# Performance work log

Measured on AMD Instinct MI355X. Metric: run time of the kernel, lower is better.

Reference implementation:

```python
import jax, jax.numpy as jnp
import numpy as np

HEAD_DIM = 8


def setup_inputs() -> dict:
    key = jax.random.key(0)
    kq, kk, k1, k2, k3, k4 = jax.random.split(key, 6)
    B, C, D, H, W = 2, 64, 32, 64, 64
    query_feats = jax.random.normal(kq, (B, C, D, H, W), dtype=jnp.float32)
    key_feats = jax.random.normal(kk, (B, C, D, H, W), dtype=jnp.float32)
    s = 1.0 / np.sqrt(C)
    # 1x1x1 Conv3d (bias=False) weights, stored as [out_ch, in_ch]
    Wq = jax.random.normal(k1, (C, C), dtype=jnp.float32) * s
    Wk = jax.random.normal(k2, (C, C), dtype=jnp.float32) * s
    Wv = jax.random.normal(k3, (C, C), dtype=jnp.float32) * s
    Wo = jax.random.normal(k4, (C, C), dtype=jnp.float32) * s
    return {"query_feats": query_feats, "key_feats": key_feats,
            "Wq": Wq, "Wk": Wk, "Wv": Wv, "Wo": Wo}


def _proj(W, x):
    # 1x1x1 conv == channel mixing
    return jnp.einsum('oc,bcdhw->bodhw', W, x)


def reference(query_feats, key_feats, Wq, Wk, Wv, Wo):
    B, C, D, H, W_ = query_feats.shape
    hw = H * W_
    heads = C // HEAD_DIM
    q = _proj(Wq, query_feats)   # [B, C, D, H, W]
    k = _proj(Wk, key_feats)
    v = _proj(Wv, key_feats)
    # reshape to [B, heads, head_dim, D, hw] then rearrange
    q = q.reshape(B, heads, HEAD_DIM, D, hw).transpose(0, 4, 1, 3, 2)  # [B,hw,heads,D,hd]
    k = k.reshape(B, heads, HEAD_DIM, D, hw).transpose(0, 4, 1, 2, 3)  # [B,hw,heads,hd,D]
    v = v.reshape(B, heads, HEAD_DIM, D, hw).transpose(0, 4, 1, 3, 2)  # [B,hw,heads,D,hd]
    sim = jnp.matmul(q, k) * (HEAD_DIM ** -0.5)      # [B,hw,heads,D,D]
    sim = jax.nn.softmax(sim, axis=-1)
    ctx = jnp.matmul(sim, v)                          # [B,hw,heads,D,hd]
    # permute(0,1,2,4,3) then flatten heads*hd -> C, then to [B,C,D,H,W]
    ctx = ctx.transpose(0, 1, 2, 4, 3).reshape(B, hw, C, D)
    ctx = ctx.transpose(0, 2, 3, 1).reshape(B, C, D, H, W_)
    out = _proj(Wo, ctx)
    return out
```

## Files before the change

### kernel.cpp

```cpp
#include <hip/hip_runtime.h>

#define SB   131072
#define CSTR 131072
#define BSTR 8388608

using u32x4  = __attribute__((ext_vector_type(4))) unsigned int;
using u32x2  = __attribute__((ext_vector_type(2))) unsigned int;
using bf16x8 = __attribute__((ext_vector_type(8))) short;
using f32x4  = __attribute__((ext_vector_type(4))) float;
using f32x2  = __attribute__((ext_vector_type(2))) float;

__device__ __forceinline__ unsigned pack2(float a, float b) {
    unsigned r;
    asm("v_cvt_pk_bf16_f32 %0, %1, %2" : "=v"(r) : "v"(a), "v"(b));
    return r;
}
__device__ __forceinline__ float bflo(unsigned u) { return __uint_as_float(u << 16); }
__device__ __forceinline__ float bfhi(unsigned u) { return __uint_as_float(u & 0xffff0000u); }

__device__ __forceinline__ f32x4 mfma16(bf16x8 a, bf16x8 b, f32x4 c) {
    return __builtin_amdgcn_mfma_f32_16x16x32_bf16(a, b, c, 0, 0, 0);
}

#define LOAD_A_FRAGS(A, W, n, qd)                                          \
    _Pragma("unroll")                                                      \
    for (int mt = 0; mt < 4; ++mt) {                                       \
        _Pragma("unroll")                                                  \
        for (int kt = 0; kt < 2; ++kt) {                                   \
            union { bf16x8 v; unsigned u[4]; } tw;                         \
            _Pragma("unroll")                                              \
            for (int r = 0; r < 4; ++r) {                                  \
                const int o = mt * 16 + (n);                               \
                const int c = kt * 32 + (qd) * 8 + 2 * r;                  \
                const float2 wv = *(const float2*)&W[o * 64 + c];          \
                tw.u[r] = pack2(wv.x, wv.y);                               \
            }                                                              \
            A[mt][kt] = tw.v;                                              \
        }                                                                  \
    }

__global__ __launch_bounds__(256)
void k1_proj(const float* __restrict__ qf, const float* __restrict__ kf,
             const float* __restrict__ Wq, const float* __restrict__ Wk,
             const float* __restrict__ Wv, unsigned* __restrict__ Qs,
             unsigned* __restrict__ Ks, unsigned* __restrict__ Vs)
{
    const int vbid = blockIdx.x >> 1;
    const int path = blockIdx.x & 1;
    const int wid  = (vbid * 256 + (int)threadIdx.x) >> 6;
    const int lane = threadIdx.x & 63;
    const int qd   = lane >> 4;
    const int n    = lane & 15;
    const int S0   = wid * 64;
    const int b    = S0 >> 17;
    const int tl   = S0 & (SB - 1);

    if (path == 0) {
        const float* xb = qf + (size_t)b * BSTR;
        bf16x8 A[4][2];
        LOAD_A_FRAGS(A, Wq, n, qd)

        #pragma unroll
        for (int t = 0; t < 4; ++t) {
            const int site = tl + t * 16 + n;
            bf16x8 Bf[2];
            #pragma unroll
            for (int kt = 0; kt < 2; ++kt) {
                union { bf16x8 v; unsigned u[4]; } tb;
                #pragma unroll
                for (int r = 0; r < 4; ++r) {
                    const int c = kt * 32 + qd * 8 + 2 * r;
                    tb.u[r] = pack2(xb[(size_t)c * CSTR + site],
                                    xb[(size_t)(c + 1) * CSTR + site]);
                }
                Bf[kt] = tb.v;
            }
            f32x4 acc[4];
            #pragma unroll
            for (int mt = 0; mt < 4; ++mt) acc[mt] = (f32x4){0.f, 0.f, 0.f, 0.f};
            #pragma unroll
            for (int kt = 0; kt < 2; ++kt)
                #pragma unroll
                for (int mt = 0; mt < 4; ++mt)
                    acc[mt] = mfma16(A[mt][kt], Bf[kt], acc[mt]);
            #pragma unroll
            for (int mt = 0; mt < 4; ++mt) {
                const int h = 2 * mt + (qd >> 1);
                unsigned* dst = Qs + ((unsigned)(b * 8 + h) * SB + site) * 4 + (qd & 1) * 2;
                u32x2 w;
                w.x = pack2(acc[mt][0], acc[mt][1]);
                w.y = pack2(acc[mt][2], acc[mt][3]);
                *(u32x2*)dst = w;
            }
        }
    } else {
        const float* xb = kf + (size_t)b * BSTR;
        bf16x8 AK[4][2], AV[4][2];
        LOAD_A_FRAGS(AK, Wk, n, qd)
        LOAD_A_FRAGS(AV, Wv, n, qd)

        #pragma unroll
        for (int t = 0; t < 4; ++t) {
            const int site = tl + t * 16 + n;
            bf16x8 Bf[2];
            #pragma unroll
            for (int kt = 0; kt < 2; ++kt) {
                union { bf16x8 v; unsigned u[4]; } tb;
                #pragma unroll
                for (int r = 0; r < 4; ++r) {
                    const int c = kt * 32 + qd * 8 + 2 * r;
                    tb.u[r] = pack2(xb[(size_t)c * CSTR + site],
                                    xb[(size_t)(c + 1) * CSTR + site]);
                }
                Bf[kt] = tb.v;
            }
            f32x4 aK[4], aV[4];
            #pragma unroll
            for (int mt = 0; mt < 4; ++mt) {
                aK[mt] = (f32x4){0.f, 0.f, 0.f, 0.f};
                aV[mt] = (f32x4){0.f, 0.f, 0.f, 0.f};
            }
            #pragma unroll
            for (int kt = 0; kt < 2; ++kt)
                #pragma unroll
                for (int mt = 0; mt < 4; ++mt) {
                    aK[mt] = mfma16(AK[mt][kt], Bf[kt], aK[mt]);
                    aV[mt] = mfma16(AV[mt][kt], Bf[kt], aV[mt]);
                }
            #pragma unroll
            for (int mt = 0; mt < 4; ++mt) {
                const int h = 2 * mt + (qd >> 1);
                const unsigned off = ((unsigned)(b * 8 + h) * SB + site) * 4 + (qd & 1) * 2;
                u32x2 wk2, wv2;
                wk2.x = pack2(aK[mt][0], aK[mt][1]);
                wk2.y = pack2(aK[mt][2], aK[mt][3]);
                wv2.x = pack2(aV[mt][0], aV[mt][1]);
                wv2.y = pack2(aV[mt][2], aV[mt][3]);
                *(u32x2*)(Ks + off) = wk2;
                *(u32x2*)(Vs + off) = wv2;
            }
        }
    }
}

__global__ __launch_bounds__(256)
void k2_attn(const u32x4* Qs, const u32x4* __restrict__ Ks,
             const u32x4* __restrict__ Vs, u32x4* Cs)
{
    __shared__ unsigned int kls[4096];
    __shared__ unsigned int vls[4096];

    const int blk = blockIdx.x;
    const int h   = blk & 7;
    const int w   = blk >> 3;
    const int b   = w >> 7;
    const int pos0 = (w & 127) * 32;

    const int tid = threadIdx.x;
    const int pos = tid & 31;
    const int dqt = tid >> 5;

    const int base = (b * 8 + h) * SB;

    #pragma unroll
    for (int i = 0; i < 4; ++i) {
        const int idx = tid + i * 256;
        const int dp = idx >> 5, pp = idx & 31;
        *(u32x4*)&kls[idx * 4] = Ks[base + dp * 4096 + pos0 + pp];
        *(u32x4*)&vls[idx * 4] = Vs[base + dp * 4096 + pos0 + pp];
    }
    __syncthreads();

    const float sc = 0.35355339059327373f * 1.4426950408889634f;

    #pragma unroll 1
    for (int p = 0; p < 2; ++p) {
        const int dq0 = dqt + 16 * p;
        const u32x4 qa = Qs[base + dq0 * 4096 + pos0 + pos];
        const u32x4 qb = Qs[base + (dq0 + 8) * 4096 + pos0 + pos];
        f32x2 q2[8];
        q2[0] = (f32x2){bflo(qa.x) * sc, bflo(qb.x) * sc};
        q2[1] = (f32x2){bfhi(qa.x) * sc, bfhi(qb.x) * sc};
        q2[2] = (f32x2){bflo(qa.y) * sc, bflo(qb.y) * sc};
        q2[3] = (f32x2){bfhi(qa.y) * sc, bfhi(qb.y) * sc};
        q2[4] = (f32x2){bflo(qa.z) * sc, bflo(qb.z) * sc};
        q2[5] = (f32x2){bfhi(qa.z) * sc, bfhi(qb.z) * sc};
        q2[6] = (f32x2){bflo(qa.w) * sc, bflo(qb.w) * sc};
        q2[7] = (f32x2){bfhi(qa.w) * sc, bfhi(qb.w) * sc};

        f32x2 cx[8];
        #pragma unroll
        for (int e = 0; e < 8; ++e) cx[e] = (f32x2){0.f, 0.f};
        f32x2 sum2 = (f32x2){0.f, 0.f};

        #pragma unroll 4
        for (int dp = 0; dp < 32; ++dp) {
            const u32x4 kk = *(const u32x4*)&kls[(dp * 32 + pos) * 4];
            const u32x4 vv = *(const u32x4*)&vls[(dp * 32 + pos) * 4];
            f32x2 accA = q2[0] * bflo(kk.x);
            f32x2 accB = q2[1] * bfhi(kk.x);
            accA += q2[2] * bflo(kk.y);
            accB += q2[3] * bfhi(kk.y);
            accA += q2[4] * bflo(kk.z);
            accB += q2[5] * bfhi(kk.z);
            accA += q2[6] * bflo(kk.w);
            accB += q2[7] * bfhi(kk.w);
            const f32x2 acc = accA + accB;
            f32x2 ex;
            ex.x = exp2f(acc.x);
            ex.y = exp2f(acc.y);
            sum2 += ex;
            cx[0] += ex * bflo(vv.x);
            cx[1] += ex * bfhi(vv.x);
            cx[2] += ex * bflo(vv.y);
            cx[3] += ex * bfhi(vv.y);
            cx[4] += ex * bflo(vv.z);
            cx[5] += ex * bfhi(vv.z);
            cx[6] += ex * bflo(vv.w);
            cx[7] += ex * bfhi(vv.w);
        }

        const f32x2 inv2 = (f32x2){1.0f / sum2.x, 1.0f / sum2.y};
        #pragma unroll
        for (int e = 0; e < 8; ++e) cx[e] *= inv2;

        u32x4 pa, pb;
        pa.x = pack2(cx[0].x, cx[1].x); pa.y = pack2(cx[2].x, cx[3].x);
        pa.z = pack2(cx[4].x, cx[5].x); pa.w = pack2(cx[6].x, cx[7].x);
        pb.x = pack2(cx[0].y, cx[1].y); pb.y = pack2(cx[2].y, cx[3].y);
        pb.z = pack2(cx[4].y, cx[5].y); pb.w = pack2(cx[6].y, cx[7].y);
        Cs[base + dq0 * 4096 + pos0 + pos] = pa;
        Cs[base + (dq0 + 8) * 4096 + pos0 + pos] = pb;
    }
}

__global__ __launch_bounds__(256)
void k3_out(const u32x4* __restrict__ Cs, const float* __restrict__ Wo,
            float* __restrict__ out)
{
    const int wid  = (blockIdx.x * 256 + threadIdx.x) >> 6;
    const int lane = threadIdx.x & 63;
    const int qd   = lane >> 4;
    const int n    = lane & 15;
    const int S0   = wid * 64;
    const int b    = S0 >> 17;
    const int tl   = S0 & (SB - 1);

    bf16x8 A[4][2];
    LOAD_A_FRAGS(A, Wo, n, qd)

    #pragma unroll
    for (int t = 0; t < 4; ++t) {
        const int site = tl + t * 16 + n;
        bf16x8 Bf[2];
        #pragma unroll
        for (int kt = 0; kt < 2; ++kt) {
            Bf[kt] = *(const bf16x8*)(Cs + (unsigned)(b * 8 + kt * 4 + qd) * SB + site);
        }
        f32x4 acc[4];
        #pragma unroll
        for (int mt = 0; mt < 4; ++mt) acc[mt] = (f32x4){0.f, 0.f, 0.f, 0.f};
        #pragma unroll
        for (int kt = 0; kt < 2; ++kt)
            #pragma unroll
            for (int mt = 0; mt < 4; ++mt)
                acc[mt] = mfma16(A[mt][kt], Bf[kt], acc[mt]);
        #pragma unroll
        for (int mt = 0; mt < 4; ++mt)
            #pragma unroll
            for (int r = 0; r < 4; ++r)
                out[(size_t)b * BSTR + (size_t)(mt * 16 + qd * 4 + r) * CSTR + site]
                    = acc[mt][r];
    }
}

extern "C" void kernel_launch(void* const* d_in, const int* in_sizes, int n_in,
                              void* d_out, int out_size, void* d_ws, size_t ws_size,
                              hipStream_t stream) {
    const float* qf = (const float*)d_in[0];
    const float* kf = (const float*)d_in[1];
    const float* Wq = (const float*)d_in[2];
    const float* Wk = (const float*)d_in[3];
    const float* Wv = (const float*)d_in[4];
    const float* Wo = (const float*)d_in[5];
    float* out = (float*)d_out;

    unsigned* Qs = (unsigned*)d_ws;
    unsigned* Vs = (unsigned*)((char*)d_ws + (size_t)33554432);
    unsigned* Ks = (unsigned*)d_out;

    hipLaunchKernelGGL(k1_proj, dim3(2048), dim3(256), 0, stream,
                       qf, kf, Wq, Wk, Wv, Qs, Ks, Vs);
    hipLaunchKernelGGL(k2_attn, dim3(2048), dim3(256), 0, stream,
                       (const u32x4*)Qs, (const u32x4*)Ks, (const u32x4*)Vs,
                       (u32x4*)Qs);
    hipLaunchKernelGGL(k3_out, dim3(1024), dim3(256), 0, stream,
                       (const u32x4*)Qs, Wo, out);
}
```

Baseline: 293.3 us.

## Stage projection input tiles into LDS via async global_load_lds and hoist loads

```diff
diff --git a/kernel.cpp b/kernel.cpp
--- a/kernel.cpp
+++ b/kernel.cpp
@@ -22,21 +22,50 @@
     return __builtin_amdgcn_mfma_f32_16x16x32_bf16(a, b, c, 0, 0, 0);
 }
 
+typedef const __attribute__((address_space(1))) void* gptr_t;
+typedef __attribute__((address_space(3))) void* lptr_t;
+__device__ __forceinline__ void gl_lds16(const float* g, float* l) {
+    __builtin_amdgcn_global_load_lds((gptr_t)g, (lptr_t)l, 16, 0, 0);
+}
+
 #define LOAD_A_FRAGS(A, W, n, qd)                                          \
     _Pragma("unroll")                                                      \
-    for (int mt = 0; mt < 4; ++mt) {                                       \
+    for (int half = 0; half < 2; ++half) {                                 \
+        float4 wr[8];                                                      \
         _Pragma("unroll")                                                  \
-        for (int kt = 0; kt < 2; ++kt) {                                   \
-            union { bf16x8 v; unsigned u[4]; } tw;                         \
+        for (int mh = 0; mh < 2; ++mh)                                     \
             _Pragma("unroll")                                              \
-            for (int r = 0; r < 4; ++r) {                                  \
-                const int o = mt * 16 + (n);                               \
-                const int c = kt * 32 + (qd) * 8 + 2 * r;                  \
-                const float2 wv = *(const float2*)&W[o * 64 + c];          \
-                tw.u[r] = pack2(wv.x, wv.y);                               \
+            for (int kt = 0; kt < 2; ++kt) {                               \
+                const int o = (half * 2 + mh) * 16 + (n);                  \
+                const int c = kt * 32 + (qd) * 8;                          \
+                wr[(mh * 2 + kt) * 2]     = *(const float4*)&W[o * 64 + c];     \
+                wr[(mh * 2 + kt) * 2 + 1] = *(const float4*)&W[o * 64 + c + 4]; \
             }                                                              \
-            A[mt][kt] = tw.v;                                              \
+        _Pragma("unroll")                                                  \
+        for (int mh = 0; mh < 2; ++mh)                                     \
+            _Pragma("unroll")                                              \
+            for (int kt = 0; kt < 2; ++kt) {                               \
+                union { bf16x8 v; unsigned u[4]; } tw;                     \
+                const float4 w0 = wr[(mh * 2 + kt) * 2];                   \
+                const float4 w1 = wr[(mh * 2 + kt) * 2 + 1];               \
+                tw.u[0] = pack2(w0.x, w0.y);                               \
+                tw.u[1] = pack2(w0.z, w0.w);                               \
+                tw.u[2] = pack2(w1.x, w1.y);                               \
+                tw.u[3] = pack2(w1.z, w1.w);                               \
+                A[half * 2 + mh][kt] = tw.v;                               \
+            }                                                              \
+    }
+
+#define LDS_BFRAG_F32(Bf, col, qd)                                         \
+    _Pragma("unroll")                                                      \
+    for (int kt = 0; kt < 2; ++kt) {                                       \
+        union { bf16x8 v; unsigned u[4]; } tb;                             \
+        _Pragma("unroll")                                                  \
+        for (int r = 0; r < 4; ++r) {                                      \
+            const int c = kt * 32 + (qd) * 8 + 2 * r;                      \
+            tb.u[r] = pack2((col)[c * 64], (col)[c * 64 + 64]);            \
         }                                                                  \
+        Bf[kt] = tb.v;                                                     \
     }
 
 __global__ __launch_bounds__(256)
@@ -45,6 +74,8 @@
              const float* __restrict__ Wv, unsigned* __restrict__ Qs,
              unsigned* __restrict__ Ks, unsigned* __restrict__ Vs)
 {
+    __shared__ float lsf[16384];
+
     const int vbid = blockIdx.x >> 1;
     const int path = blockIdx.x & 1;
     const int wid  = (vbid * 256 + (int)threadIdx.x) >> 6;
@@ -54,27 +85,31 @@
     const int S0   = wid * 64;
     const int b    = S0 >> 17;
     const int tl   = S0 & (SB - 1);
+    const int woff = ((int)threadIdx.x >> 6) * 4096;
+
+    const float* xb = (path == 0 ? qf : kf) + (size_t)b * BSTR;
+
+    {
+        const float* gsrc = xb + (size_t)(lane >> 4) * CSTR + tl + (lane & 15) * 4;
+        float* ldst = &lsf[woff];
+        #pragma unroll
+        for (int i = 0; i < 16; ++i)
+            gl_lds16(gsrc + (size_t)(4 * i) * CSTR, ldst + i * 256);
+    }
 
     if (path == 0) {
-        const float* xb = qf + (size_t)b * BSTR;
         bf16x8 A[4][2];
         LOAD_A_FRAGS(A, Wq, n, qd)
+        asm volatile("s_waitcnt vmcnt(0)" ::: "memory");
+        __builtin_amdgcn_sched_barrier(0);
 
         #pragma unroll
         for (int t = 0; t < 4; ++t) {
-            const int site = tl + t * 16 + n;
+            const int sl   = t * 16 + n;
+            const int site = tl + sl;
+            const float* col = &lsf[woff + sl];
             bf16x8 Bf[2];
-            #pragma unroll
-            for (int kt = 0; kt < 2; ++kt) {
-                union { bf16x8 v; unsigned u[4]; } tb;
-                #pragma unroll
-                for (int r = 0; r < 4; ++r) {
-                    const int c = kt * 32 + qd * 8 + 2 * r;
-                    tb.u[r] = pack2(xb[(size_t)c * CSTR + site],
-                                    xb[(size_t)(c + 1) * CSTR + site]);
-                }
-                Bf[kt] = tb.v;
-            }
+            LDS_BFRAG_F32(Bf, col, qd)
             f32x4 acc[4];
             #pragma unroll
             for (int mt = 0; mt < 4; ++mt) acc[mt] = (f32x4){0.f, 0.f, 0.f, 0.f};
@@ -94,26 +129,19 @@
             }
         }
     } else {
-        const float* xb = kf + (size_t)b * BSTR;
         bf16x8 AK[4][2], AV[4][2];
         LOAD_A_FRAGS(AK, Wk, n, qd)
         LOAD_A_FRAGS(AV, Wv, n, qd)
+        asm volatile("s_waitcnt vmcnt(0)" ::: "memory");
+        __builtin_amdgcn_sched_barrier(0);
 
         #pragma unroll
         for (int t = 0; t < 4; ++t) {
-            const int site = tl + t * 16 + n;
+            const int sl   = t * 16 + n;
+            const int site = tl + sl;
+            const float* col = &lsf[woff + sl];
             bf16x8 Bf[2];
-            #pragma unroll
-            for (int kt = 0; kt < 2; ++kt) {
-                union { bf16x8 v; unsigned u[4]; } tb;
-                #pragma unroll
-                for (int r = 0; r < 4; ++r) {
-                    const int c = kt * 32 + qd * 8 + 2 * r;
-                    tb.u[r] = pack2(xb[(size_t)c * CSTR + site],
-                                    xb[(size_t)(c + 1) * CSTR + site]);
-                }
-                Bf[kt] = tb.v;
-            }
+            LDS_BFRAG_F32(Bf, col, qd)
             f32x4 aK[4], aV[4];
             #pragma unroll
             for (int mt = 0; mt < 4; ++mt) {
@@ -246,17 +274,21 @@
     const int b    = S0 >> 17;
     const int tl   = S0 & (SB - 1);
 
-    bf16x8 A[4][2];
-    LOAD_A_FRAGS(A, Wo, n, qd)
-
+    bf16x8 Bf[4][2];
     #pragma unroll
     for (int t = 0; t < 4; ++t) {
         const int site = tl + t * 16 + n;
-        bf16x8 Bf[2];
-        #pragma unroll
-        for (int kt = 0; kt < 2; ++kt) {
-            Bf[kt] = *(const bf16x8*)(Cs + (unsigned)(b * 8 + kt * 4 + qd) * SB + site);
-        }
+        #pragma unroll
+        for (int kt = 0; kt < 2; ++kt)
+            Bf[t][kt] = *(const bf16x8*)(Cs + (unsigned)(b * 8 + kt * 4 + qd) * SB + site);
+    }
+
+    bf16x8 A[4][2];
+    LOAD_A_FRAGS(A, Wo, n, qd)
+
+    #pragma unroll
+    for (int t = 0; t < 4; ++t) {
+        const int site = tl + t * 16 + n;
         f32x4 acc[4];
         #pragma unroll
         for (int mt = 0; mt < 4; ++mt) acc[mt] = (f32x4){0.f, 0.f, 0.f, 0.f};
@@ -264,7 +296,7 @@
         for (int kt = 0; kt < 2; ++kt)
             #pragma unroll
             for (int mt = 0; mt < 4; ++mt)
-                acc[mt] = mfma16(A[mt][kt], Bf[kt], acc[mt]);
+                acc[mt] = mfma16(A[mt][kt], Bf[t][kt], acc[mt]);
         #pragma unroll
         for (int mt = 0; mt < 4; ++mt)
             #pragma unroll
```

Result: no change. 292.1 us (-0.4%).
